# Optimization experiments

Measured on AMD Instinct MI355X. Metric: run time of the kernel, lower is better.

Reference implementation:

```python
import jax, jax.numpy as jnp
import numpy as np

B, S, D, H = 4, 2048, 1024, 16
HD = D // H  # head_dim = 64


def setup_inputs() -> dict:
    key = jax.random.key(0)
    ks = jax.random.split(key, 5)
    s = 1.0 / np.sqrt(D)
    return {
        "x": jax.random.normal(ks[0], (B, S, D), jnp.float32),
        "Wq": jax.random.normal(ks[1], (D, D), jnp.float32) * s,
        "Wk": jax.random.normal(ks[2], (D, D), jnp.float32) * s,
        "Wv": jax.random.normal(ks[3], (D, D), jnp.float32) * s,
        "Wo": jax.random.normal(ks[4], (D, D), jnp.float32) * s,
        "bo": jnp.zeros((D,), jnp.float32),
    }


def reference(x, Wq, Wk, Wv, Wo, bo):
    b, s, d = x.shape
    # projections (torch Linear: x @ W.T; weights here stored as [in, out] equivalent)
    q = (x @ Wq).reshape(b, s, H, HD).transpose(0, 2, 1, 3)  # [b,h,s,hd]
    k = (x @ Wk).reshape(b, s, H, HD).transpose(0, 2, 1, 3)
    v = (x @ Wv).reshape(b, s, H, HD).transpose(0, 2, 1, 3)
    scores = jnp.einsum("bhqd,bhkd->bhqk", q, k) * (HD ** -0.5)
    causal = jnp.tril(jnp.ones((s, s), bool))  # mask==0 -> -inf
    scores = jnp.where(causal, scores, -jnp.inf)
    attn = jax.nn.softmax(scores, axis=-1)
    out = jnp.einsum("bhqk,bhkd->bhqd", attn, v)
    out = out.transpose(0, 2, 1, 3).reshape(b, s, d)
    return out @ Wo + bo
```

## Files before the change

### kernel.cpp

```cpp
#include <hip/hip_runtime.h>
#include <cstdint>
#include <cstddef>

typedef __attribute__((ext_vector_type(8))) short bf16x8;
typedef __attribute__((ext_vector_type(4))) short bf16x4;
typedef __attribute__((ext_vector_type(4))) float f32x4;

constexpr int Bsz = 4, Ssz = 2048, Dsz = 1024, Hn = 16, HDsz = 64;
constexpr int Msz = Bsz * Ssz;
constexpr float LOG2E = 1.4426950408889634f;

#define MFMA16(a, b, c) __builtin_amdgcn_mfma_f32_16x16x16bf16_1k(a, b, c, 0, 0, 0)

__device__ __forceinline__ unsigned short f2bf(float f) {
  union { float f; unsigned int u; } v; v.f = f;
  unsigned int r = v.u + 0x7fffu + ((v.u >> 16) & 1u);
  return (unsigned short)(r >> 16);
}

typedef __attribute__((address_space(1))) const unsigned int gu32;
typedef __attribute__((address_space(3))) unsigned int lu32;
__device__ __forceinline__ void async_cp16(const unsigned short* g, unsigned short* l) {
  __builtin_amdgcn_global_load_lds((gu32*)g, (lu32*)l, 16, 0, 0);
}

__global__ void cvt_bf16_kernel(const float* __restrict__ in,
                                unsigned short* __restrict__ out, int n4) {
  int i = blockIdx.x * blockDim.x + threadIdx.x;
  if (i >= n4) return;
  const float4 v = reinterpret_cast<const float4*>(in)[i];
  ushort4 o;
  o.x = f2bf(v.x); o.y = f2bf(v.y); o.z = f2bf(v.z); o.w = f2bf(v.w);
  reinterpret_cast<ushort4*>(out)[i] = o;
}

__global__ void cvt_transpose4_kernel(const float* __restrict__ W0, const float* __restrict__ W1,
                                      const float* __restrict__ W2, const float* __restrict__ W3,
                                      unsigned short* __restrict__ T0, unsigned short* __restrict__ T1,
                                      unsigned short* __restrict__ T2, unsigned short* __restrict__ T3) {
  __shared__ float tile[32][33];
  const int z = blockIdx.z;
  const float* W = (z == 0) ? W0 : (z == 1) ? W1 : (z == 2) ? W2 : W3;
  unsigned short* Wt = (z == 0) ? T0 : (z == 1) ? T1 : (z == 2) ? T2 : T3;
  int tx = threadIdx.x & 31, ty = threadIdx.x >> 5;
  int bx = blockIdx.x, by = blockIdx.y;
#pragma unroll
  for (int i = 0; i < 4; i++) {
    int k = by * 32 + ty + i * 8;
    tile[ty + i * 8][tx] = W[k * Dsz + bx * 32 + tx];
  }
  __syncthreads();
#pragma unroll
  for (int i = 0; i < 4; i++) {
    int nrow = bx * 32 + ty + i * 8;
    Wt[nrow * Dsz + by * 32 + tx] = f2bf(tile[tx][ty + i * 8]);
  }
}

enum { EPI_QKV = 0, EPI_OUT = 1 };

template <int EPI>
__global__ __launch_bounds__(256)
void gemm_bk64(const unsigned short* __restrict__ A,
               const unsigned short* __restrict__ Bt,
               unsigned short* __restrict__ Qh,
               unsigned short* __restrict__ Kh,
               unsigned short* __restrict__ Vth,
               float* __restrict__ Out,
               const float* __restrict__ bias) {
  __shared__ unsigned short As[128 * 64];
  __shared__ unsigned short Bs[128 * 64];

  const int tid = threadIdx.x;
  const int w = tid >> 6, lane = tid & 63;
  const int l15 = lane & 15, quad = lane >> 4;
  const int wr = w >> 1, wc = w & 1;
  const int bm = blockIdx.y, bn = blockIdx.x;
  const int rr = lane >> 3;
  const int scoff = ((lane & 7) ^ rr) * 8;

  f32x4 acc[4][4];
#pragma unroll
  for (int i = 0; i < 4; i++)
#pragma unroll
    for (int j = 0; j < 4; j++) acc[i][j] = (f32x4){0.f, 0.f, 0.f, 0.f};

  const int rowA0 = bm * 128, rowB0 = bn * 128;

  for (int kt = 0; kt < Dsz / 64; kt++) {
#pragma unroll
    for (int i = 0; i < 4; i++) {
      const int r8 = w * 32 + i * 8;
      async_cp16(&A[(size_t)(rowA0 + r8 + rr) * Dsz + kt * 64 + scoff], &As[r8 * 64]);
      async_cp16(&Bt[(size_t)(rowB0 + r8 + rr) * Dsz + kt * 64 + scoff], &Bs[r8 * 64]);
    }
    __syncthreads();

#pragma unroll
    for (int ks = 0; ks < 2; ks++) {
      bf16x8 af[4], bfr[4];
#pragma unroll
      for (int t = 0; t < 4; t++) {
        const int ra = wr * 64 + t * 16 + l15;
        af[t] = *reinterpret_cast<const bf16x8*>(
            &As[ra * 64 + (((ks * 4 + quad) ^ (ra & 7)) * 8)]);
        const int rb = wc * 64 + t * 16 + l15;
        bfr[t] = *reinterpret_cast<const bf16x8*>(
            &Bs[rb * 64 + (((ks * 4 + quad) ^ (rb & 7)) * 8)]);
      }
#pragma unroll
      for (int i = 0; i < 4; i++)
#pragma unroll
        for (int j = 0; j < 4; j++)
          acc[i][j] = __builtin_amdgcn_mfma_f32_16x16x32_bf16(af[i], bfr[j], acc[i][j], 0, 0, 0);
    }
    __syncthreads();
  }

  if (EPI == EPI_QKV) {
    const int proj = (bn * 128) >> 10;
#pragma unroll
    for (int i = 0; i < 4; i++) {
#pragma unroll
      for (int j = 0; j < 4; j++) {
        const int n = bn * 128 + wc * 64 + j * 16 + l15;
        const int nn = n & 1023, h = nn >> 6, hd = nn & 63;
        const int m0 = bm * 128 + wr * 64 + i * 16 + quad * 4;
        const int b = m0 >> 11, s0 = m0 & (Ssz - 1);
        if (proj == 0) {
#pragma unroll
          for (int r = 0; r < 4; r++)
            Qh[((size_t)(b * Hn + h) * Ssz + s0 + r) * HDsz + hd] =
                f2bf(acc[i][j][r] * (0.125f * LOG2E));
        } else if (proj == 1) {
#pragma unroll
          for (int r = 0; r < 4; r++)
            Kh[((size_t)(b * Hn + h) * Ssz + s0 + r) * HDsz + hd] = f2bf(acc[i][j][r]);
        } else {
          ushort4 o;
          o.x = f2bf(acc[i][j][0]); o.y = f2bf(acc[i][j][1]);
          o.z = f2bf(acc[i][j][2]); o.w = f2bf(acc[i][j][3]);
          *reinterpret_cast<ushort4*>(
              &Vth[((size_t)(b * Hn + h) * HDsz + hd) * Ssz + s0]) = o;
        }
      }
    }
  } else {
#pragma unroll
    for (int i = 0; i < 4; i++) {
#pragma unroll
      for (int j = 0; j < 4; j++) {
        const int n = bn * 128 + wc * 64 + j * 16 + l15;
        const int m0 = bm * 128 + wr * 64 + i * 16 + quad * 4;
#pragma unroll
        for (int r = 0; r < 4; r++)
          Out[(size_t)(m0 + r) * Dsz + n] = acc[i][j][r] + bias[n];
      }
    }
  }
}

__global__ __launch_bounds__(256)
void flash_kernel(const unsigned short* __restrict__ Q,
                  const unsigned short* __restrict__ Kg,
                  const unsigned short* __restrict__ Vt,
                  unsigned short* __restrict__ AO) {
  __shared__ unsigned short Ks[64 * 64];
  __shared__ unsigned short Vs[64 * 64];

  const int tid = threadIdx.x;
  const int w = tid >> 6, lane = tid & 63;
  const int l15 = lane & 15, quad = lane >> 4;
  const int rr = lane >> 3;
  const int scoff = ((lane & 7) ^ rr) * 8;

  const int linear = blockIdx.y * 8 + blockIdx.x;
  const int bh = (linear & 7) * 8 + ((linear >> 3) & 7);
  const int p = linear >> 6;

  const unsigned short* Qb = Q + (size_t)bh * Ssz * HDsz;
  const unsigned short* Kb = Kg + (size_t)bh * Ssz * HDsz;
  const unsigned short* Vb = Vt + (size_t)bh * HDsz * Ssz;
  const int b = bh / Hn, h = bh % Hn;

  for (int ph = 0; ph < 2; ph++) {
    const int t = ph ? (15 - p) : p;
    const int q0 = t * 128;
    const int rowStart = q0 + w * 32;

    bf16x8 qf[2][2];
#pragma unroll
    for (int tm = 0; tm < 2; tm++)
#pragma unroll
      for (int ks = 0; ks < 2; ks++)
        qf[tm][ks] = *reinterpret_cast<const bf16x8*>(
            &Qb[(size_t)(rowStart + tm * 16 + l15) * HDsz + ks * 32 + quad * 8]);

    f32x4 oacc[2][4];
    float lpart[2] = {0.f, 0.f};
#pragma unroll
    for (int tm = 0; tm < 2; tm++)
#pragma unroll
      for (int tn = 0; tn < 4; tn++) oacc[tm][tn] = (f32x4){0.f, 0.f, 0.f, 0.f};

    const int nkb = 2 * t + 2;
    for (int kb = 0; kb < nkb; kb++) {
      const int kv0 = kb * 64;
#pragma unroll
      for (int i = 0; i < 2; i++) {
        const int r8 = w * 16 + i * 8;
        async_cp16(&Kb[(size_t)(kv0 + r8 + rr) * HDsz + scoff], &Ks[r8 * 64]);
        async_cp16(&Vb[(size_t)(r8 + rr) * Ssz + kv0 + scoff], &Vs[r8 * 64]);
      }
      __syncthreads();

      const bool skip = (kv0 >= rowStart + 32);
      if (!skip) {
        f32x4 sc[4][2];
#pragma unroll
        for (int tn = 0; tn < 4; tn++)
#pragma unroll
          for (int tm = 0; tm < 2; tm++) sc[tn][tm] = (f32x4){0.f, 0.f, 0.f, 0.f};
#pragma unroll
        for (int ks = 0; ks < 2; ks++) {
#pragma unroll
          for (int tn = 0; tn < 4; tn++) {
            const int rk = tn * 16 + l15;
            bf16x8 kf = *reinterpret_cast<const bf16x8*>(
                &Ks[rk * 64 + (((ks * 4 + quad) ^ (rk & 7)) * 8)]);
#pragma unroll
            for (int tm = 0; tm < 2; tm++)
              sc[tn][tm] = __builtin_amdgcn_mfma_f32_16x16x32_bf16(kf, qf[tm][ks], sc[tn][tm], 0, 0, 0);
          }
        }

        const bool needMask = (kv0 + 63 > rowStart);
        if (needMask) {
#pragma unroll
          for (int tn = 0; tn < 4; tn++)
#pragma unroll
            for (int tm = 0; tm < 2; tm++) {
              const int qrow = rowStart + tm * 16 + l15;
#pragma unroll
              for (int r = 0; r < 4; r++)
                if (kv0 + tn * 16 + quad * 4 + r > qrow) sc[tn][tm][r] = -1e30f;
            }
        }

        unsigned int pk[4][2][2];
#pragma unroll
        for (int tn = 0; tn < 4; tn++)
#pragma unroll
          for (int tm = 0; tm < 2; tm++) {
            union { float f; unsigned int u; } e0, e1, e2, e3;
            e0.f = __builtin_amdgcn_exp2f(sc[tn][tm][0]);
            e1.f = __builtin_amdgcn_exp2f(sc[tn][tm][1]);
            e2.f = __builtin_amdgcn_exp2f(sc[tn][tm][2]);
            e3.f = __builtin_amdgcn_exp2f(sc[tn][tm][3]);
            lpart[tm] += (e0.f + e1.f) + (e2.f + e3.f);
            pk[tn][tm][0] = __builtin_amdgcn_perm(e1.u, e0.u, 0x07060302u);
            pk[tn][tm][1] = __builtin_amdgcn_perm(e3.u, e2.u, 0x07060302u);
          }

#pragma unroll
        for (int tn = 0; tn < 4; tn++) {
          bf16x4 pa[2];
#pragma unroll
          for (int tm = 0; tm < 2; tm++) {
            union { unsigned int u[2]; bf16x4 v; } cv;
            cv.u[0] = pk[tn][tm][0]; cv.u[1] = pk[tn][tm][1];
            pa[tm] = cv.v;
          }
#pragma unroll
          for (int to = 0; to < 4; to++) {
            const int rv = to * 16 + l15;
            const int chunk = tn * 2 + (quad >> 1);
            bf16x4 vf = *reinterpret_cast<const bf16x4*>(
                (const char*)Vs + rv * 128 + ((chunk ^ (rv & 7)) * 16) + (quad & 1) * 8);
#pragma unroll
            for (int tm = 0; tm < 2; tm++)
              oacc[tm][to] = MFMA16(pa[tm], vf, oacc[tm][to]);
          }
        }
      }
      __syncthreads();
    }

#pragma unroll
    for (int tm = 0; tm < 2; tm++) {
      float lf = lpart[tm];
      lf += __shfl_xor(lf, 16);
      lf += __shfl_xor(lf, 32);
      float linv[4];
#pragma unroll
      for (int r = 0; r < 4; r++) {
        union { float f; int i; } cv;
        cv.f = lf;
        cv.i = __builtin_amdgcn_ds_bpermute((quad * 4 + r) * 4, cv.i);
        linv[r] = 1.f / cv.f;
      }
#pragma unroll
      for (int r = 0; r < 4; r++) {
        const int s = rowStart + tm * 16 + quad * 4 + r;
        const size_t m = (size_t)b * Ssz + s;
#pragma unroll
        for (int tn = 0; tn < 4; tn++) {
          const int n = h * HDsz + tn * 16 + l15;
          AO[m * Dsz + n] = f2bf(oacc[tm][tn][r] * linv[r]);
        }
      }
      lpart[tm] = 0.f;
    }
  }
}

extern "C" void kernel_launch(void* const* d_in, const int* in_sizes, int n_in,
                              void* d_out, int out_size, void* d_ws, size_t ws_size,
                              hipStream_t stream) {
  const float* x  = (const float*)d_in[0];
  const float* Wq = (const float*)d_in[1];
  const float* Wk = (const float*)d_in[2];
  const float* Wv = (const float*)d_in[3];
  const float* Wo = (const float*)d_in[4];
  const float* bo = (const float*)d_in[5];
  float* out = (float*)d_out;

  unsigned short* xb  = (unsigned short*)d_ws;
  unsigned short* Wqt = xb + (size_t)Msz * Dsz;
  unsigned short* Wkt = Wqt + (size_t)Dsz * Dsz;
  unsigned short* Wvt = Wkt + (size_t)Dsz * Dsz;
  unsigned short* Wot = Wvt + (size_t)Dsz * Dsz;
  unsigned short* Qh  = Wot + (size_t)Dsz * Dsz;
  unsigned short* Kh  = Qh + (size_t)Msz * Dsz;
  unsigned short* Vth = Kh + (size_t)Msz * Dsz;
  unsigned short* AO  = Vth + (size_t)Msz * Dsz;

  cvt_bf16_kernel<<<(Msz * Dsz / 4 + 255) / 256, 256, 0, stream>>>(x, xb, Msz * Dsz / 4);
  cvt_transpose4_kernel<<<dim3(Dsz / 32, Dsz / 32, 4), 256, 0, stream>>>(
      Wq, Wk, Wv, Wo, Wqt, Wkt, Wvt, Wot);

  gemm_bk64<EPI_QKV><<<dim3(3 * Dsz / 128, Msz / 128), 256, 0, stream>>>(
      xb, Wqt, Qh, Kh, Vth, nullptr, nullptr);

  flash_kernel<<<dim3(8, Bsz * Hn), 256, 0, stream>>>(Qh, Kh, Vth, AO);

  gemm_bk64<EPI_OUT><<<dim3(Dsz / 128, Msz / 128), 256, 0, stream>>>(
      AO, Wot, nullptr, nullptr, nullptr, out, bo);
}
```

Measured before the change: 249.3 us.

## Use 8-wave GEMM blocks and 64-row flash attention query tiles

The projection GEMMs now run 512 threads per 128x128 tile, with each of eight waves owning a 32x64 sub-tile. Per-thread accumulators and loads are halved, so more waves are resident to hide latency. The flash kernel now processes 64-row query tiles, one 16-row slice per wave, over twice as many blocks, and only the diagonal key block is masked. This cuts wasted causal work and improves load balance, but each K/V tile loaded into LDS is reused by fewer query rows.

```diff
diff --git a/kernel.cpp b/kernel.cpp
--- a/kernel.cpp
+++ b/kernel.cpp
@@ -60,7 +60,7 @@
 enum { EPI_QKV = 0, EPI_OUT = 1 };
 
 template <int EPI>
-__global__ __launch_bounds__(256)
+__global__ __launch_bounds__(512, 4)
 void gemm_bk64(const unsigned short* __restrict__ A,
                const unsigned short* __restrict__ Bt,
                unsigned short* __restrict__ Qh,
@@ -79,9 +79,9 @@
   const int rr = lane >> 3;
   const int scoff = ((lane & 7) ^ rr) * 8;
 
-  f32x4 acc[4][4];
-#pragma unroll
-  for (int i = 0; i < 4; i++)
+  f32x4 acc[2][4];
+#pragma unroll
+  for (int i = 0; i < 2; i++)
 #pragma unroll
     for (int j = 0; j < 4; j++) acc[i][j] = (f32x4){0.f, 0.f, 0.f, 0.f};
 
@@ -89,8 +89,8 @@
 
   for (int kt = 0; kt < Dsz / 64; kt++) {
 #pragma unroll
-    for (int i = 0; i < 4; i++) {
-      const int r8 = w * 32 + i * 8;
+    for (int i = 0; i < 2; i++) {
+      const int r8 = w * 16 + i * 8;
       async_cp16(&A[(size_t)(rowA0 + r8 + rr) * Dsz + kt * 64 + scoff], &As[r8 * 64]);
       async_cp16(&Bt[(size_t)(rowB0 + r8 + rr) * Dsz + kt * 64 + scoff], &Bs[r8 * 64]);
     }
@@ -98,18 +98,21 @@
 
 #pragma unroll
     for (int ks = 0; ks < 2; ks++) {
-      bf16x8 af[4], bfr[4];
-#pragma unroll
-      for (int t = 0; t < 4; t++) {
-        const int ra = wr * 64 + t * 16 + l15;
+      bf16x8 af[2], bfr[4];
+#pragma unroll
+      for (int t = 0; t < 2; t++) {
+        const int ra = wr * 32 + t * 16 + l15;
         af[t] = *reinterpret_cast<const bf16x8*>(
             &As[ra * 64 + (((ks * 4 + quad) ^ (ra & 7)) * 8)]);
+      }
+#pragma unroll
+      for (int t = 0; t < 4; t++) {
         const int rb = wc * 64 + t * 16 + l15;
         bfr[t] = *reinterpret_cast<const bf16x8*>(
             &Bs[rb * 64 + (((ks * 4 + quad) ^ (rb & 7)) * 8)]);
       }
 #pragma unroll
-      for (int i = 0; i < 4; i++)
+      for (int i = 0; i < 2; i++)
 #pragma unroll
         for (int j = 0; j < 4; j++)
           acc[i][j] = __builtin_amdgcn_mfma_f32_16x16x32_bf16(af[i], bfr[j], acc[i][j], 0, 0, 0);
@@ -120,12 +123,12 @@
   if (EPI == EPI_QKV) {
     const int proj = (bn * 128) >> 10;
 #pragma unroll
-    for (int i = 0; i < 4; i++) {
+    for (int i = 0; i < 2; i++) {
 #pragma unroll
       for (int j = 0; j < 4; j++) {
         const int n = bn * 128 + wc * 64 + j * 16 + l15;
         const int nn = n & 1023, h = nn >> 6, hd = nn & 63;
-        const int m0 = bm * 128 + wr * 64 + i * 16 + quad * 4;
+        const int m0 = bm * 128 + wr * 32 + i * 16 + quad * 4;
         const int b = m0 >> 11, s0 = m0 & (Ssz - 1);
         if (proj == 0) {
 #pragma unroll
@@ -147,11 +150,11 @@
     }
   } else {
 #pragma unroll
-    for (int i = 0; i < 4; i++) {
+    for (int i = 0; i < 2; i++) {
 #pragma unroll
       for (int j = 0; j < 4; j++) {
         const int n = bn * 128 + wc * 64 + j * 16 + l15;
-        const int m0 = bm * 128 + wr * 64 + i * 16 + quad * 4;
+        const int m0 = bm * 128 + wr * 32 + i * 16 + quad * 4;
 #pragma unroll
         for (int r = 0; r < 4; r++)
           Out[(size_t)(m0 + r) * Dsz + n] = acc[i][j][r] + bias[n];
@@ -174,7 +177,7 @@
   const int rr = lane >> 3;
   const int scoff = ((lane & 7) ^ rr) * 8;
 
-  const int linear = blockIdx.y * 8 + blockIdx.x;
+  const int linear = blockIdx.y * 16 + blockIdx.x;
   const int bh = (linear & 7) * 8 + ((linear >> 3) & 7);
   const int p = linear >> 6;
 
@@ -184,27 +187,22 @@
   const int b = bh / Hn, h = bh % Hn;
 
   for (int ph = 0; ph < 2; ph++) {
-    const int t = ph ? (15 - p) : p;
-    const int q0 = t * 128;
-    const int rowStart = q0 + w * 32;
-
-    bf16x8 qf[2][2];
-#pragma unroll
-    for (int tm = 0; tm < 2; tm++)
-#pragma unroll
-      for (int ks = 0; ks < 2; ks++)
-        qf[tm][ks] = *reinterpret_cast<const bf16x8*>(
-            &Qb[(size_t)(rowStart + tm * 16 + l15) * HDsz + ks * 32 + quad * 8]);
-
-    f32x4 oacc[2][4];
-    float lpart[2] = {0.f, 0.f};
-#pragma unroll
-    for (int tm = 0; tm < 2; tm++)
-#pragma unroll
-      for (int tn = 0; tn < 4; tn++) oacc[tm][tn] = (f32x4){0.f, 0.f, 0.f, 0.f};
-
-    const int nkb = 2 * t + 2;
-    for (int kb = 0; kb < nkb; kb++) {
+    const int t = ph ? (31 - p) : p;
+    const int q0 = t * 64;
+    const int rowStart = q0 + w * 16;
+
+    bf16x8 qf[2];
+#pragma unroll
+    for (int ks = 0; ks < 2; ks++)
+      qf[ks] = *reinterpret_cast<const bf16x8*>(
+          &Qb[(size_t)(rowStart + l15) * HDsz + ks * 32 + quad * 8]);
+
+    f32x4 oacc[4];
+    float lpart = 0.f;
+#pragma unroll
+    for (int tn = 0; tn < 4; tn++) oacc[tn] = (f32x4){0.f, 0.f, 0.f, 0.f};
+
+    for (int kb = 0; kb <= t; kb++) {
       const int kv0 = kb * 64;
 #pragma unroll
       for (int i = 0; i < 2; i++) {
@@ -214,102 +212,79 @@
       }
       __syncthreads();
 
-      const bool skip = (kv0 >= rowStart + 32);
-      if (!skip) {
-        f32x4 sc[4][2];
+      f32x4 sc[4];
+#pragma unroll
+      for (int tn = 0; tn < 4; tn++) sc[tn] = (f32x4){0.f, 0.f, 0.f, 0.f};
+#pragma unroll
+      for (int ks = 0; ks < 2; ks++) {
+#pragma unroll
+        for (int tn = 0; tn < 4; tn++) {
+          const int rk = tn * 16 + l15;
+          bf16x8 kf = *reinterpret_cast<const bf16x8*>(
+              &Ks[rk * 64 + (((ks * 4 + quad) ^ (rk & 7)) * 8)]);
+          sc[tn] = __builtin_amdgcn_mfma_f32_16x16x32_bf16(kf, qf[ks], sc[tn], 0, 0, 0);
+        }
+      }
+
+      if (kb == t) {
+        const int qrel = w * 16 + l15;
 #pragma unroll
         for (int tn = 0; tn < 4; tn++)
 #pragma unroll
-          for (int tm = 0; tm < 2; tm++) sc[tn][tm] = (f32x4){0.f, 0.f, 0.f, 0.f};
-#pragma unroll
-        for (int ks = 0; ks < 2; ks++) {
-#pragma unroll
-          for (int tn = 0; tn < 4; tn++) {
-            const int rk = tn * 16 + l15;
-            bf16x8 kf = *reinterpret_cast<const bf16x8*>(
-                &Ks[rk * 64 + (((ks * 4 + quad) ^ (rk & 7)) * 8)]);
-#pragma unroll
-            for (int tm = 0; tm < 2; tm++)
-              sc[tn][tm] = __builtin_amdgcn_mfma_f32_16x16x32_bf16(kf, qf[tm][ks], sc[tn][tm], 0, 0, 0);
-          }
+          for (int r = 0; r < 4; r++)
+            if (tn * 16 + quad * 4 + r > qrel) sc[tn][r] = -1e30f;
+      }
+
+      unsigned int pk[4][2];
+#pragma unroll
+      for (int tn = 0; tn < 4; tn++) {
+        union { float f; unsigned int u; } e0, e1, e2, e3;
+        e0.f = __builtin_amdgcn_exp2f(sc[tn][0]);
+        e1.f = __builtin_amdgcn_exp2f(sc[tn][1]);
+        e2.f = __builtin_amdgcn_exp2f(sc[tn][2]);
+        e3.f = __builtin_amdgcn_exp2f(sc[tn][3]);
+        lpart += (e0.f + e1.f) + (e2.f + e3.f);
+        pk[tn][0] = __builtin_amdgcn_perm(e1.u, e0.u, 0x07060302u);
+        pk[tn][1] = __builtin_amdgcn_perm(e3.u, e2.u, 0x07060302u);
+      }
+
+#pragma unroll
+      for (int tn = 0; tn < 4; tn++) {
+        union { unsigned int u[2]; bf16x4 v; } cv;
+        cv.u[0] = pk[tn][0]; cv.u[1] = pk[tn][1];
+        const bf16x4 pa = cv.v;
+#pragma unroll
+        for (int to = 0; to < 4; to++) {
+          const int rv = to * 16 + l15;
+          const int chunk = tn * 2 + (quad >> 1);
+          bf16x4 vf = *reinterpret_cast<const bf16x4*>(
+              (const char*)Vs + rv * 128 + ((chunk ^ (rv & 7)) * 16) + (quad & 1) * 8);
+          oacc[to] = MFMA16(pa, vf, oacc[to]);
         }
-
-        const bool needMask = (kv0 + 63 > rowStart);
-        if (needMask) {
-#pragma unroll
-          for (int tn = 0; tn < 4; tn++)
-#pragma unroll
-            for (int tm = 0; tm < 2; tm++) {
-              const int qrow = rowStart + tm * 16 + l15;
-#pragma unroll
-              for (int r = 0; r < 4; r++)
-                if (kv0 + tn * 16 + quad * 4 + r > qrow) sc[tn][tm][r] = -1e30f;
-            }
-        }
-
-        unsigned int pk[4][2][2];
-#pragma unroll
-        for (int tn = 0; tn < 4; tn++)
-#pragma unroll
-          for (int tm = 0; tm < 2; tm++) {
-            union { float f; unsigned int u; } e0, e1, e2, e3;
-            e0.f = __builtin_amdgcn_exp2f(sc[tn][tm][0]);
-            e1.f = __builtin_amdgcn_exp2f(sc[tn][tm][1]);
-            e2.f = __builtin_amdgcn_exp2f(sc[tn][tm][2]);
-            e3.f = __builtin_amdgcn_exp2f(sc[tn][tm][3]);
-            lpart[tm] += (e0.f + e1.f) + (e2.f + e3.f);
-            pk[tn][tm][0] = __builtin_amdgcn_perm(e1.u, e0.u, 0x07060302u);
-            pk[tn][tm][1] = __builtin_amdgcn_perm(e3.u, e2.u, 0x07060302u);
-          }
-
-#pragma unroll
-        for (int tn = 0; tn < 4; tn++) {
-          bf16x4 pa[2];
-#pragma unroll
-          for (int tm = 0; tm < 2; tm++) {
-            union { unsigned int u[2]; bf16x4 v; } cv;
-            cv.u[0] = pk[tn][tm][0]; cv.u[1] = pk[tn][tm][1];
-            pa[tm] = cv.v;
-          }
-#pragma unroll
-          for (int to = 0; to < 4; to++) {
-            const int rv = to * 16 + l15;
-            const int chunk = tn * 2 + (quad >> 1);
-            bf16x4 vf = *reinterpret_cast<const bf16x4*>(
-                (const char*)Vs + rv * 128 + ((chunk ^ (rv & 7)) * 16) + (quad & 1) * 8);
-#pragma unroll
-            for (int tm = 0; tm < 2; tm++)
-              oacc[tm][to] = MFMA16(pa[tm], vf, oacc[tm][to]);
-          }
-        }
       }
       __syncthreads();
     }
 
-#pragma unroll
-    for (int tm = 0; tm < 2; tm++) {
-      float lf = lpart[tm];
-      lf += __shfl_xor(lf, 16);
-      lf += __shfl_xor(lf, 32);
-      float linv[4];
-#pragma unroll
-      for (int r = 0; r < 4; r++) {
-        union { float f; int i; } cv;
-        cv.f = lf;
-        cv.i = __builtin_amdgcn_ds_bpermute((quad * 4 + r) * 4, cv.i);
-        linv[r] = 1.f / cv.f;
-      }
-#pragma unroll
-      for (int r = 0; r < 4; r++) {
-        const int s = rowStart + tm * 16 + quad * 4 + r;
-        const size_t m = (size_t)b * Ssz + s;
-#pragma unroll
-        for (int tn = 0; tn < 4; tn++) {
-          const int n = h * HDsz + tn * 16 + l15;
-          AO[m * Dsz + n] = f2bf(oacc[tm][tn][r] * linv[r]);
-        }
-      }
-      lpart[tm] = 0.f;
+    float lf = lpart;
+    lf += __shfl_xor(lf, 16);
+    lf += __shfl_xor(lf, 32);
+    float linv[4];
+#pragma unroll
+    for (int r = 0; r < 4; r++) {
+      union { float f; int i; } cv;
+      cv.f = lf;
+      cv.i = __builtin_amdgcn_ds_bpermute((quad * 4 + r) * 4, cv.i);
+      linv[r] = 1.f / cv.f;
+    }
+#pragma unroll
+    for (int r = 0; r < 4; r++) {
+      const int s = rowStart + quad * 4 + r;
+      const size_t m = (size_t)b * Ssz + s;
+#pragma unroll
+      for (int tn = 0; tn < 4; tn++) {
+        const int n = h * HDsz + tn * 16 + l15;
+        AO[m * Dsz + n] = f2bf(oacc[tn][r] * linv[r]);
+      }
     }
   }
 }
@@ -339,11 +314,11 @@
   cvt_transpose4_kernel<<<dim3(Dsz / 32, Dsz / 32, 4), 256, 0, stream>>>(
       Wq, Wk, Wv, Wo, Wqt, Wkt, Wvt, Wot);
 
-  gemm_bk64<EPI_QKV><<<dim3(3 * Dsz / 128, Msz / 128), 256, 0, stream>>>(
+  gemm_bk64<EPI_QKV><<<dim3(3 * Dsz / 128, Msz / 128), 512, 0, stream>>>(
       xb, Wqt, Qh, Kh, Vth, nullptr, nullptr);
 
-  flash_kernel<<<dim3(8, Bsz * Hn), 256, 0, stream>>>(Qh, Kh, Vth, AO);
-
-  gemm_bk64<EPI_OUT><<<dim3(Dsz / 128, Msz / 128), 256, 0, stream>>>(
+  flash_kernel<<<dim3(16, Bsz * Hn), 256, 0, stream>>>(Qh, Kh, Vth, AO);
+
+  gemm_bk64<EPI_OUT><<<dim3(Dsz / 128, Msz / 128), 512, 0, stream>>>(
       AO, Wot, nullptr, nullptr, nullptr, out, bo);
 }
```

Measured after the change: 237.0 us. 1.05x faster.
